# Kernel optimization log

Hardware: AMD Instinct MI355X
Metric: run time of the kernel (lower is better)

Reference implementation:

```python
import jax, jax.numpy as jnp
import numpy as np

BN_EPS = 1e-5
NORM_EPS = 1e-12  # torch F.normalize eps


def setup_inputs() -> dict:
    key = jax.random.key(0)
    ks = jax.random.split(key, 7)
    B, N, D, K = 32, 4096, 512, 64
    init_sc = 1.0 / np.sqrt(D)
    x = jax.random.normal(ks[0], (B, N, D), dtype=jnp.float32)
    clusters = init_sc * jax.random.normal(ks[1], (D, K), dtype=jnp.float32)
    clusters2 = init_sc * jax.random.normal(ks[2], (1, D, K), dtype=jnp.float32)
    bn_weight = jax.random.uniform(ks[3], (K,), dtype=jnp.float32, minval=0.5, maxval=1.5)
    bn_bias = 0.1 * jax.random.normal(ks[4], (K,), dtype=jnp.float32)
    running_mean = 0.1 * jax.random.normal(ks[5], (K,), dtype=jnp.float32)
    running_var = jax.random.uniform(ks[6], (K,), dtype=jnp.float32, minval=0.5, maxval=1.5)
    return {"x": x, "clusters": clusters, "clusters2": clusters2,
            "bn_weight": bn_weight, "bn_bias": bn_bias,
            "running_mean": running_mean, "running_var": running_var}


def reference(x, clusters, clusters2, bn_weight, bn_bias, running_mean, running_var):
    B, N, D = x.shape
    K = clusters2.shape[2]
    x_flat = x.reshape(-1, D)                              # (B*N) x D
    logits = x_flat @ clusters                             # (B*N) x (K+G)
    # BatchNorm1d in eval mode: use running stats
    inv_std = jax.lax.rsqrt(running_var + BN_EPS)
    logits = (logits - running_mean) * inv_std * bn_weight + bn_bias
    assignment = jax.nn.softmax(logits, axis=1)[:, :K]     # drop ghost clusters
    assignment = assignment.reshape(B, N, K)
    a_sum = assignment.sum(axis=1, keepdims=True)
    a = a_sum * clusters2                                  # B x D x K
    vlad = jnp.einsum('bnk,bnd->bdk', assignment, x) - a   # B x D x K
    # intra-normalization over D (torch F.normalize dim=1)
    vlad = vlad / jnp.maximum(jnp.linalg.norm(vlad, axis=1, keepdims=True), NORM_EPS)
    vlad = vlad.reshape(B, D * K)
    vlad = vlad / jnp.maximum(jnp.linalg.norm(vlad, axis=1, keepdims=True), NORM_EPS)
    return vlad
```

## Files before the change

### kernel.cpp

```cpp
#include <hip/hip_runtime.h>

#define B_ 32
#define N_ 4096
#define D_ 512
#define K_ 64

__global__ __launch_bounds__(256) void k_assign(
    const float* __restrict__ x, const float* __restrict__ clusters,
    const float* __restrict__ bnw, const float* __restrict__ bnb,
    const float* __restrict__ rm, const float* __restrict__ rv,
    float* __restrict__ asg, float* __restrict__ a_sum)
{
    const int tid = threadIdx.x;
    const int tx = tid & 15, ty = tid >> 4;
    const int r0 = blockIdx.x * 64;
    const int b  = r0 >> 12;

    __shared__ __align__(16) float xs[32][68];
    __shared__ __align__(16) float cs[32][68];
    __shared__ float red[16][64];

    float acc[4][4] = {};

    for (int k0 = 0; k0 < D_; k0 += 32) {
        #pragma unroll
        for (int l = 0; l < 2; ++l) {
            int idx = tid + (l << 8);
            int row = idx >> 3;
            int kk4 = (idx & 7) << 2;
            const float4 v = *(const float4*)&x[(size_t)(r0 + row) * D_ + k0 + kk4];
            xs[kk4 + 0][row] = v.x;
            xs[kk4 + 1][row] = v.y;
            xs[kk4 + 2][row] = v.z;
            xs[kk4 + 3][row] = v.w;
        }
        #pragma unroll
        for (int l = 0; l < 2; ++l) {
            int idx = tid + (l << 8);
            int kk  = idx >> 4;
            int c4  = (idx & 15) << 2;
            *(float4*)&cs[kk][c4] = *(const float4*)&clusters[(size_t)(k0 + kk) * K_ + c4];
        }
        __syncthreads();
        #pragma unroll
        for (int kk = 0; kk < 32; ++kk) {
            const float4 xv = *(const float4*)&xs[kk][ty << 2];
            const float4 cv = *(const float4*)&cs[kk][tx << 2];
            const float xa[4] = {xv.x, xv.y, xv.z, xv.w};
            const float ca[4] = {cv.x, cv.y, cv.z, cv.w};
            #pragma unroll
            for (int i = 0; i < 4; ++i)
                #pragma unroll
                for (int j = 0; j < 4; ++j)
                    acc[i][j] = fmaf(xa[i], ca[j], acc[i][j]);
        }
        __syncthreads();
    }

    const float4 w4 = *(const float4*)&bnw[tx << 2];
    const float4 b4 = *(const float4*)&bnb[tx << 2];
    const float4 m4 = *(const float4*)&rm[tx << 2];
    const float4 v4 = *(const float4*)&rv[tx << 2];
    const float wa[4] = {w4.x, w4.y, w4.z, w4.w};
    const float ba[4] = {b4.x, b4.y, b4.z, b4.w};
    const float ma[4] = {m4.x, m4.y, m4.z, m4.w};
    const float va[4] = {v4.x, v4.y, v4.z, v4.w};
    float alpha[4], beta[4];
    #pragma unroll
    for (int j = 0; j < 4; ++j) {
        alpha[j] = wa[j] * rsqrtf(va[j] + 1e-5f);
        beta[j]  = ba[j] - ma[j] * alpha[j];
    }

    float rs[4] = {0.f, 0.f, 0.f, 0.f};
    #pragma unroll
    for (int i = 0; i < 4; ++i) {
        float lg[4];
        #pragma unroll
        for (int j = 0; j < 4; ++j) lg[j] = fmaf(acc[i][j], alpha[j], beta[j]);
        float mx = fmaxf(fmaxf(lg[0], lg[1]), fmaxf(lg[2], lg[3]));
        #pragma unroll
        for (int msk = 1; msk <= 8; msk <<= 1) mx = fmaxf(mx, __shfl_xor(mx, msk));
        float e[4];
        float s = 0.f;
        #pragma unroll
        for (int j = 0; j < 4; ++j) { e[j] = __expf(lg[j] - mx); s += e[j]; }
        #pragma unroll
        for (int msk = 1; msk <= 8; msk <<= 1) s += __shfl_xor(s, msk);
        const float invs = 1.0f / s;
        float4 o;
        o.x = e[0] * invs; o.y = e[1] * invs; o.z = e[2] * invs; o.w = e[3] * invs;
        const int row = (ty << 2) + i;
        *(float4*)&asg[(size_t)(r0 + row) * K_ + (tx << 2)] = o;
        rs[0] += o.x; rs[1] += o.y; rs[2] += o.z; rs[3] += o.w;
    }

    *(float4*)&red[ty][tx << 2] = make_float4(rs[0], rs[1], rs[2], rs[3]);
    __syncthreads();
    if (tid < 64) {
        float s = 0.f;
        #pragma unroll
        for (int t2 = 0; t2 < 16; ++t2) s += red[t2][tid];
        atomicAdd(&a_sum[(b << 6) + tid], s);
    }
}

__global__ __launch_bounds__(256) void k_vlad(
    const float* __restrict__ x, const float* __restrict__ asg,
    float* __restrict__ part)
{
    const int tid = threadIdx.x;
    const int tx = tid & 15, ty = tid >> 4;
    const int s  = blockIdx.x;
    const int dt = blockIdx.y;
    const int b  = blockIdx.z;
    const int d0 = dt << 6;
    const int n0 = s << 10;

    __shared__ __align__(16) float xt[32][68];
    __shared__ __align__(16) float at[32][68];

    float acc[4][4] = {};

    for (int nc = 0; nc < 32; ++nc) {
        const int nb = n0 + (nc << 5);
        #pragma unroll
        for (int l = 0; l < 2; ++l) {
            int idx = tid + (l << 8);
            int nn  = idx >> 4;
            int d4  = (idx & 15) << 2;
            *(float4*)&xt[nn][d4] =
                *(const float4*)&x[(size_t)(b * N_ + nb + nn) * D_ + d0 + d4];
        }
        #pragma unroll
        for (int l = 0; l < 2; ++l) {
            int idx = tid + (l << 8);
            int nn  = idx >> 4;
            int k4  = (idx & 15) << 2;
            *(float4*)&at[nn][k4] =
                *(const float4*)&asg[(size_t)(b * N_ + nb + nn) * K_ + k4];
        }
        __syncthreads();
        #pragma unroll
        for (int nn = 0; nn < 32; ++nn) {
            const float4 xv = *(const float4*)&xt[nn][ty << 2];
            const float4 av = *(const float4*)&at[nn][tx << 2];
            const float xa[4] = {xv.x, xv.y, xv.z, xv.w};
            const float aa[4] = {av.x, av.y, av.z, av.w};
            #pragma unroll
            for (int i = 0; i < 4; ++i)
                #pragma unroll
                for (int j = 0; j < 4; ++j)
                    acc[i][j] = fmaf(xa[i], aa[j], acc[i][j]);
        }
        __syncthreads();
    }

    #pragma unroll
    for (int i = 0; i < 4; ++i) {
        const size_t off =
            ((size_t)(s * B_ + b) * D_ + d0 + (ty << 2) + i) * K_ + (tx << 2);
        *(float4*)&part[off] = make_float4(acc[i][0], acc[i][1], acc[i][2], acc[i][3]);
    }
}

__global__ __launch_bounds__(256) void k_final1(
    const float* __restrict__ part, const float* __restrict__ a_sum,
    const float* __restrict__ c2, float* __restrict__ out,
    float* __restrict__ ssqk)
{
    const int b  = blockIdx.x;
    const int dc = blockIdx.y;
    const int t  = threadIdx.x;
    const int k  = t & 63, g = t >> 6;
    __shared__ float sp[4][64];

    const float  ak = a_sum[(b << 6) + k];
    const size_t bo = (size_t)b * D_ * K_;
    const size_t PS = (size_t)B_ * D_ * K_;
    float ssq = 0.f;
    const int dlo = (dc << 7) + (g << 5);
    for (int d = dlo; d < dlo + 32; ++d) {
        const size_t off = ((size_t)d << 6) + k;
        float v = part[bo + off] + part[PS + bo + off]
                + part[2 * PS + bo + off] + part[3 * PS + bo + off];
        v = fmaf(-ak, c2[off], v);
        out[((size_t)b << 15) + off] = v;
        ssq = fmaf(v, v, ssq);
    }
    sp[g][k] = ssq;
    __syncthreads();
    if (t < 64)
        atomicAdd(&ssqk[(b << 6) + t], sp[0][t] + sp[1][t] + sp[2][t] + sp[3][t]);
}

__global__ __launch_bounds__(256) void k_final2(
    const float* __restrict__ ssqk, float* __restrict__ out)
{
    const int b  = blockIdx.x;
    const int dc = blockIdx.y;
    const int t  = threadIdx.x;
    const int k  = t & 63, g = t >> 6;
    __shared__ float invk_s[64];
    __shared__ float invg_s;

    if (t < 64) {
        const float s   = ssqk[(b << 6) + t];
        const float inv = 1.0f / fmaxf(sqrtf(s), 1e-12f);
        invk_s[t] = inv;
        float gp = s * inv * inv;
        #pragma unroll
        for (int m = 1; m < 64; m <<= 1) gp += __shfl_xor(gp, m);
        if (t == 0) invg_s = 1.0f / fmaxf(sqrtf(gp), 1e-12f);
    }
    __syncthreads();
    const float scale = invk_s[k] * invg_s;
    const int dlo = (dc << 7) + (g << 5);
    for (int d = dlo; d < dlo + 32; ++d) {
        const size_t off = ((size_t)b << 15) + ((size_t)d << 6) + k;
        out[off] *= scale;
    }
}

extern "C" void kernel_launch(void* const* d_in, const int* in_sizes, int n_in,
                              void* d_out, int out_size, void* d_ws, size_t ws_size,
                              hipStream_t stream)
{
    const float* x    = (const float*)d_in[0];
    const float* clus = (const float*)d_in[1];
    const float* c2   = (const float*)d_in[2];
    const float* bnw  = (const float*)d_in[3];
    const float* bnb  = (const float*)d_in[4];
    const float* rm   = (const float*)d_in[5];
    const float* rv   = (const float*)d_in[6];
    float* out = (float*)d_out;

    float* asg   = (float*)d_ws;
    float* a_sum = asg + (size_t)B_ * N_ * K_;
    float* ssqk  = a_sum + B_ * K_;
    float* part  = ssqk + B_ * K_;

    hipMemsetAsync(a_sum, 0, 2 * B_ * K_ * sizeof(float), stream);

    k_assign<<<dim3(B_ * N_ / 64), 256, 0, stream>>>(x, clus, bnw, bnb, rm, rv, asg, a_sum);
    k_vlad<<<dim3(4, 8, B_), 256, 0, stream>>>(x, asg, part);
    k_final1<<<dim3(B_, 4), 256, 0, stream>>>(part, a_sum, c2, out, ssqk);
    k_final2<<<dim3(B_, 4), 256, 0, stream>>>(ssqk, out);
}
```

Baseline: 543.3 us.

## Use split-bf16 MFMA for both GEMMs with transposed packed assignment buffer

```diff
diff --git a/kernel.cpp b/kernel.cpp
--- a/kernel.cpp
+++ b/kernel.cpp
@@ -1,224 +1,319 @@
 #include <hip/hip_runtime.h>
+#include <stdint.h>
 
 #define B_ 32
 #define N_ 4096
 #define D_ 512
 #define K_ 64
+#define M_ (B_ * N_)
+#define NSPLIT 8
+
+typedef float f32x4 __attribute__((ext_vector_type(4)));
+typedef short bf16x8 __attribute__((ext_vector_type(8)));
+typedef uint32_t u32;
+
+union U8 { u32 u[4]; bf16x8 v; uint4 q4; };
+
+__device__ __forceinline__ u32 pack_hi2(float a, float b) {
+    return __builtin_amdgcn_perm(__float_as_uint(b), __float_as_uint(a), 0x07060302u);
+}
+__device__ __forceinline__ u32 lo16s(u32 p0, u32 p1) {
+    return __builtin_amdgcn_perm(p1, p0, 0x05040100u);
+}
+__device__ __forceinline__ u32 hi16s(u32 p0, u32 p1) {
+    return __builtin_amdgcn_perm(p1, p0, 0x07060302u);
+}
+__device__ __forceinline__ float trunc_hi(float f) {
+    return __uint_as_float(__float_as_uint(f) & 0xffff0000u);
+}
+
+__global__ void k_prep(const float* __restrict__ clusters,
+                       bf16x8* __restrict__ cfh, bf16x8* __restrict__ cfl)
+{
+    const int t = blockIdx.x;
+    const int c = blockIdx.y;
+    const int lane = threadIdx.x;
+    const int q = lane >> 4, li = lane & 15;
+    U8 h, l;
+    #pragma unroll
+    for (int j2 = 0; j2 < 4; ++j2) {
+        float v0 = clusters[(t*32 + q*8 + 2*j2 + 0) * K_ + c*16 + li];
+        float v1 = clusters[(t*32 + q*8 + 2*j2 + 1) * K_ + c*16 + li];
+        float l0 = v0 - trunc_hi(v0), l1 = v1 - trunc_hi(v1);
+        h.u[j2] = pack_hi2(v0, v1);
+        l.u[j2] = pack_hi2(l0, l1);
+    }
+    cfh[(t*4 + c)*64 + lane] = h.v;
+    cfl[(t*4 + c)*64 + lane] = l.v;
+}
 
 __global__ __launch_bounds__(256) void k_assign(
-    const float* __restrict__ x, const float* __restrict__ clusters,
+    const float* __restrict__ x,
+    const bf16x8* __restrict__ cfh, const bf16x8* __restrict__ cfl,
     const float* __restrict__ bnw, const float* __restrict__ bnb,
     const float* __restrict__ rm, const float* __restrict__ rv,
-    float* __restrict__ asg, float* __restrict__ a_sum)
+    u32* __restrict__ asgT, float* __restrict__ a_sum)
 {
     const int tid = threadIdx.x;
-    const int tx = tid & 15, ty = tid >> 4;
-    const int r0 = blockIdx.x * 64;
-    const int b  = r0 >> 12;
-
-    __shared__ __align__(16) float xs[32][68];
-    __shared__ __align__(16) float cs[32][68];
-    __shared__ float red[16][64];
-
-    float acc[4][4] = {};
-
-    for (int k0 = 0; k0 < D_; k0 += 32) {
-        #pragma unroll
-        for (int l = 0; l < 2; ++l) {
-            int idx = tid + (l << 8);
-            int row = idx >> 3;
-            int kk4 = (idx & 7) << 2;
-            const float4 v = *(const float4*)&x[(size_t)(r0 + row) * D_ + k0 + kk4];
-            xs[kk4 + 0][row] = v.x;
-            xs[kk4 + 1][row] = v.y;
-            xs[kk4 + 2][row] = v.z;
-            xs[kk4 + 3][row] = v.w;
-        }
-        #pragma unroll
-        for (int l = 0; l < 2; ++l) {
-            int idx = tid + (l << 8);
-            int kk  = idx >> 4;
-            int c4  = (idx & 15) << 2;
-            *(float4*)&cs[kk][c4] = *(const float4*)&clusters[(size_t)(k0 + kk) * K_ + c4];
-        }
-        __syncthreads();
-        #pragma unroll
-        for (int kk = 0; kk < 32; ++kk) {
-            const float4 xv = *(const float4*)&xs[kk][ty << 2];
-            const float4 cv = *(const float4*)&cs[kk][tx << 2];
-            const float xa[4] = {xv.x, xv.y, xv.z, xv.w};
-            const float ca[4] = {cv.x, cv.y, cv.z, cv.w};
-            #pragma unroll
-            for (int i = 0; i < 4; ++i)
-                #pragma unroll
-                for (int j = 0; j < 4; ++j)
-                    acc[i][j] = fmaf(xa[i], ca[j], acc[i][j]);
-        }
-        __syncthreads();
-    }
-
-    const float4 w4 = *(const float4*)&bnw[tx << 2];
-    const float4 b4 = *(const float4*)&bnb[tx << 2];
-    const float4 m4 = *(const float4*)&rm[tx << 2];
-    const float4 v4 = *(const float4*)&rv[tx << 2];
-    const float wa[4] = {w4.x, w4.y, w4.z, w4.w};
-    const float ba[4] = {b4.x, b4.y, b4.z, b4.w};
-    const float ma[4] = {m4.x, m4.y, m4.z, m4.w};
-    const float va[4] = {v4.x, v4.y, v4.z, v4.w};
+    const int w = tid >> 6, lane = tid & 63;
+    const int q = lane >> 4, li = lane & 15;
+    const int rbase = blockIdx.x * 128 + w * 32;
+
+    __shared__ __align__(16) u32 asgT_lds[64][132];
+    __shared__ float red[4][64];
+
+    f32x4 acc[2][4];
+    #pragma unroll
+    for (int i = 0; i < 2; ++i)
+        #pragma unroll
+        for (int j = 0; j < 4; ++j) acc[i][j] = (f32x4){0.f, 0.f, 0.f, 0.f};
+
+    for (int t = 0; t < 16; ++t) {
+        bf16x8 bh[4], bl[4];
+        #pragma unroll
+        for (int c = 0; c < 4; ++c) {
+            bh[c] = cfh[(t*4 + c)*64 + lane];
+            bl[c] = cfl[(t*4 + c)*64 + lane];
+        }
+        #pragma unroll
+        for (int mt = 0; mt < 2; ++mt) {
+            const float* xp = x + (size_t)(rbase + mt*16 + li) * D_ + t*32 + q*8;
+            float v[8];
+            *(float4*)&v[0] = *(const float4*)xp;
+            *(float4*)&v[4] = *(const float4*)(xp + 4);
+            float lo[8];
+            #pragma unroll
+            for (int j = 0; j < 8; ++j) lo[j] = v[j] - trunc_hi(v[j]);
+            U8 ah, al;
+            #pragma unroll
+            for (int j2 = 0; j2 < 4; ++j2) {
+                ah.u[j2] = pack_hi2(v[2*j2], v[2*j2+1]);
+                al.u[j2] = pack_hi2(lo[2*j2], lo[2*j2+1]);
+            }
+            #pragma unroll
+            for (int c = 0; c < 4; ++c) {
+                acc[mt][c] = __builtin_amdgcn_mfma_f32_16x16x32_bf16(ah.v, bh[c], acc[mt][c], 0, 0, 0);
+                acc[mt][c] = __builtin_amdgcn_mfma_f32_16x16x32_bf16(ah.v, bl[c], acc[mt][c], 0, 0, 0);
+                acc[mt][c] = __builtin_amdgcn_mfma_f32_16x16x32_bf16(al.v, bh[c], acc[mt][c], 0, 0, 0);
+            }
+        }
+    }
+
     float alpha[4], beta[4];
     #pragma unroll
-    for (int j = 0; j < 4; ++j) {
-        alpha[j] = wa[j] * rsqrtf(va[j] + 1e-5f);
-        beta[j]  = ba[j] - ma[j] * alpha[j];
+    for (int c = 0; c < 4; ++c) {
+        const int col = c*16 + li;
+        const float a = bnw[col] * rsqrtf(rv[col] + 1e-5f);
+        alpha[c] = a;
+        beta[c]  = bnb[col] - rm[col] * a;
     }
 
     float rs[4] = {0.f, 0.f, 0.f, 0.f};
     #pragma unroll
-    for (int i = 0; i < 4; ++i) {
-        float lg[4];
-        #pragma unroll
-        for (int j = 0; j < 4; ++j) lg[j] = fmaf(acc[i][j], alpha[j], beta[j]);
-        float mx = fmaxf(fmaxf(lg[0], lg[1]), fmaxf(lg[2], lg[3]));
-        #pragma unroll
-        for (int msk = 1; msk <= 8; msk <<= 1) mx = fmaxf(mx, __shfl_xor(mx, msk));
-        float e[4];
-        float s = 0.f;
-        #pragma unroll
-        for (int j = 0; j < 4; ++j) { e[j] = __expf(lg[j] - mx); s += e[j]; }
-        #pragma unroll
-        for (int msk = 1; msk <= 8; msk <<= 1) s += __shfl_xor(s, msk);
-        const float invs = 1.0f / s;
-        float4 o;
-        o.x = e[0] * invs; o.y = e[1] * invs; o.z = e[2] * invs; o.w = e[3] * invs;
-        const int row = (ty << 2) + i;
-        *(float4*)&asg[(size_t)(r0 + row) * K_ + (tx << 2)] = o;
-        rs[0] += o.x; rs[1] += o.y; rs[2] += o.z; rs[3] += o.w;
-    }
-
-    *(float4*)&red[ty][tx << 2] = make_float4(rs[0], rs[1], rs[2], rs[3]);
+    for (int mt = 0; mt < 2; ++mt) {
+        u32 pr[4][4];
+        #pragma unroll
+        for (int reg = 0; reg < 4; ++reg) {
+            float lg[4];
+            #pragma unroll
+            for (int c = 0; c < 4; ++c) lg[c] = fmaf(acc[mt][c][reg], alpha[c], beta[c]);
+            float mx = fmaxf(fmaxf(lg[0], lg[1]), fmaxf(lg[2], lg[3]));
+            #pragma unroll
+            for (int m = 1; m <= 8; m <<= 1) mx = fmaxf(mx, __shfl_xor(mx, m));
+            float e[4], s = 0.f;
+            #pragma unroll
+            for (int c = 0; c < 4; ++c) { e[c] = __expf(lg[c] - mx); s += e[c]; }
+            #pragma unroll
+            for (int m = 1; m <= 8; m <<= 1) s += __shfl_xor(s, m);
+            const float inv = 1.0f / s;
+            #pragma unroll
+            for (int c = 0; c < 4; ++c) {
+                const float a = e[c] * inv;
+                rs[c] += a;
+                const float alo = a - trunc_hi(a);
+                pr[reg][c] = pack_hi2(a, alo);
+            }
+        }
+        #pragma unroll
+        for (int c = 0; c < 4; ++c) {
+            *(uint4*)&asgT_lds[c*16 + li][w*32 + mt*16 + q*4] =
+                make_uint4(pr[0][c], pr[1][c], pr[2][c], pr[3][c]);
+        }
+    }
+
+    #pragma unroll
+    for (int c = 0; c < 4; ++c) {
+        rs[c] += __shfl_xor(rs[c], 16);
+        rs[c] += __shfl_xor(rs[c], 32);
+    }
+    if (q == 0) {
+        #pragma unroll
+        for (int c = 0; c < 4; ++c) red[w][c*16 + li] = rs[c];
+    }
     __syncthreads();
     if (tid < 64) {
-        float s = 0.f;
-        #pragma unroll
-        for (int t2 = 0; t2 < 16; ++t2) s += red[t2][tid];
-        atomicAdd(&a_sum[(b << 6) + tid], s);
+        const float s = red[0][tid] + red[1][tid] + red[2][tid] + red[3][tid];
+        atomicAdd(&a_sum[(blockIdx.x >> 5) * K_ + tid], s);
+    }
+
+    const size_t ncol0 = (size_t)blockIdx.x * 128;
+    #pragma unroll
+    for (int l = 0; l < 8; ++l) {
+        const int ii = tid + 256*l;
+        const int k = ii >> 5, seg = ii & 31;
+        const uint4 vv = *(const uint4*)&asgT_lds[k][seg*4];
+        *(uint4*)&asgT[(size_t)k * M_ + ncol0 + seg*4] = vv;
     }
 }
 
 __global__ __launch_bounds__(256) void k_vlad(
-    const float* __restrict__ x, const float* __restrict__ asg,
+    const float* __restrict__ x, const u32* __restrict__ asgT,
     float* __restrict__ part)
 {
     const int tid = threadIdx.x;
-    const int tx = tid & 15, ty = tid >> 4;
+    const int w = tid >> 6, lane = tid & 63;
+    const int q = lane >> 4, li = lane & 15;
     const int s  = blockIdx.x;
-    const int dt = blockIdx.y;
+    const int db = blockIdx.y;
     const int b  = blockIdx.z;
-    const int d0 = dt << 6;
-    const int n0 = s << 10;
-
-    __shared__ __align__(16) float xt[32][68];
-    __shared__ __align__(16) float at[32][68];
-
-    float acc[4][4] = {};
-
-    for (int nc = 0; nc < 32; ++nc) {
-        const int nb = n0 + (nc << 5);
-        #pragma unroll
-        for (int l = 0; l < 2; ++l) {
-            int idx = tid + (l << 8);
-            int nn  = idx >> 4;
-            int d4  = (idx & 15) << 2;
-            *(float4*)&xt[nn][d4] =
-                *(const float4*)&x[(size_t)(b * N_ + nb + nn) * D_ + d0 + d4];
-        }
-        #pragma unroll
-        for (int l = 0; l < 2; ++l) {
-            int idx = tid + (l << 8);
-            int nn  = idx >> 4;
-            int k4  = (idx & 15) << 2;
-            *(float4*)&at[nn][k4] =
-                *(const float4*)&asg[(size_t)(b * N_ + nb + nn) * K_ + k4];
-        }
-        __syncthreads();
-        #pragma unroll
-        for (int nn = 0; nn < 32; ++nn) {
-            const float4 xv = *(const float4*)&xt[nn][ty << 2];
-            const float4 av = *(const float4*)&at[nn][tx << 2];
-            const float xa[4] = {xv.x, xv.y, xv.z, xv.w};
-            const float aa[4] = {av.x, av.y, av.z, av.w};
-            #pragma unroll
-            for (int i = 0; i < 4; ++i)
-                #pragma unroll
-                for (int j = 0; j < 4; ++j)
-                    acc[i][j] = fmaf(xa[i], aa[j], acc[i][j]);
-        }
-        __syncthreads();
-    }
-
+    const int d0 = db*256 + w*64;
+    const int nbb = b * N_ + s * (N_ / NSPLIT);
+
+    f32x4 acc[4][4];
+    #pragma unroll
+    for (int i = 0; i < 4; ++i)
+        #pragma unroll
+        for (int j = 0; j < 4; ++j) acc[i][j] = (f32x4){0.f, 0.f, 0.f, 0.f};
+
+    for (int ch = 0; ch < (N_ / NSPLIT) / 32; ++ch) {
+        const int nb = ch*32 + q*8;
+        bf16x8 ah[4], al[4];
+        #pragma unroll
+        for (int mt = 0; mt < 4; ++mt) {
+            const u32* ap = asgT + (size_t)(mt*16 + li) * M_ + nbb + nb;
+            u32 p[8];
+            *(uint4*)&p[0] = *(const uint4*)ap;
+            *(uint4*)&p[4] = *(const uint4*)(ap + 4);
+            U8 uh, ul;
+            #pragma unroll
+            for (int j2 = 0; j2 < 4; ++j2) {
+                uh.u[j2] = lo16s(p[2*j2], p[2*j2+1]);
+                ul.u[j2] = hi16s(p[2*j2], p[2*j2+1]);
+            }
+            ah[mt] = uh.v; al[mt] = ul.v;
+        }
+        #pragma unroll
+        for (int nt = 0; nt < 4; ++nt) {
+            const float* xp = x + (size_t)(nbb + nb) * D_ + d0 + nt*16 + li;
+            float v[8];
+            #pragma unroll
+            for (int j = 0; j < 8; ++j) v[j] = xp[(size_t)j * D_];
+            float lo[8];
+            #pragma unroll
+            for (int j = 0; j < 8; ++j) lo[j] = v[j] - trunc_hi(v[j]);
+            U8 bh, bl;
+            #pragma unroll
+            for (int j2 = 0; j2 < 4; ++j2) {
+                bh.u[j2] = pack_hi2(v[2*j2], v[2*j2+1]);
+                bl.u[j2] = pack_hi2(lo[2*j2], lo[2*j2+1]);
+            }
+            #pragma unroll
+            for (int mt = 0; mt < 4; ++mt) {
+                acc[mt][nt] = __builtin_amdgcn_mfma_f32_16x16x32_bf16(ah[mt], bh.v, acc[mt][nt], 0, 0, 0);
+                acc[mt][nt] = __builtin_amdgcn_mfma_f32_16x16x32_bf16(ah[mt], bl.v, acc[mt][nt], 0, 0, 0);
+                acc[mt][nt] = __builtin_amdgcn_mfma_f32_16x16x32_bf16(al[mt], bh.v, acc[mt][nt], 0, 0, 0);
+            }
+        }
+    }
+
+    float* pp = part + ((size_t)s * B_ + b) * ((size_t)K_ * D_);
+    #pragma unroll
+    for (int mt = 0; mt < 4; ++mt)
+        #pragma unroll
+        for (int nt = 0; nt < 4; ++nt) {
+            const int d = d0 + nt*16 + li;
+            #pragma unroll
+            for (int reg = 0; reg < 4; ++reg) {
+                const int k = mt*16 + q*4 + reg;
+                pp[(size_t)k * D_ + d] = acc[mt][nt][reg];
+            }
+        }
+}
+
+__global__ __launch_bounds__(256) void k_final1(
+    const float* __restrict__ part_ro, const float* __restrict__ a_sum,
+    const float* __restrict__ c2, float* __restrict__ part0,
+    float* __restrict__ ssqk)
+{
+    const int b = blockIdx.x, dc = blockIdx.y;
+    const int tid = threadIdx.x;
+    const int k = tid >> 2, ds = tid & 3;
+    const int d0 = dc*64 + ds*16;
+    const float ak = a_sum[b*K_ + k];
+    const size_t PS = (size_t)B_ * K_ * D_;
+    const size_t base = ((size_t)b * K_ + k) * D_ + d0;
+    float ssq = 0.f;
     #pragma unroll
     for (int i = 0; i < 4; ++i) {
-        const size_t off =
-            ((size_t)(s * B_ + b) * D_ + d0 + (ty << 2) + i) * K_ + (tx << 2);
-        *(float4*)&part[off] = make_float4(acc[i][0], acc[i][1], acc[i][2], acc[i][3]);
-    }
-}
-
-__global__ __launch_bounds__(256) void k_final1(
-    const float* __restrict__ part, const float* __restrict__ a_sum,
-    const float* __restrict__ c2, float* __restrict__ out,
-    float* __restrict__ ssqk)
-{
-    const int b  = blockIdx.x;
-    const int dc = blockIdx.y;
-    const int t  = threadIdx.x;
-    const int k  = t & 63, g = t >> 6;
-    __shared__ float sp[4][64];
-
-    const float  ak = a_sum[(b << 6) + k];
-    const size_t bo = (size_t)b * D_ * K_;
-    const size_t PS = (size_t)B_ * D_ * K_;
-    float ssq = 0.f;
-    const int dlo = (dc << 7) + (g << 5);
-    for (int d = dlo; d < dlo + 32; ++d) {
-        const size_t off = ((size_t)d << 6) + k;
-        float v = part[bo + off] + part[PS + bo + off]
-                + part[2 * PS + bo + off] + part[3 * PS + bo + off];
-        v = fmaf(-ak, c2[off], v);
-        out[((size_t)b << 15) + off] = v;
-        ssq = fmaf(v, v, ssq);
-    }
-    sp[g][k] = ssq;
+        float4 v = *(const float4*)(part_ro + base + i*4);
+        #pragma unroll
+        for (int s = 1; s < NSPLIT; ++s) {
+            const float4 p = *(const float4*)(part_ro + s*PS + base + i*4);
+            v.x += p.x; v.y += p.y; v.z += p.z; v.w += p.w;
+        }
+        const int d = d0 + i*4;
+        v.x = fmaf(-ak, c2[(d+0)*K_ + k], v.x);
+        v.y = fmaf(-ak, c2[(d+1)*K_ + k], v.y);
+        v.z = fmaf(-ak, c2[(d+2)*K_ + k], v.z);
+        v.w = fmaf(-ak, c2[(d+3)*K_ + k], v.w);
+        ssq = fmaf(v.x, v.x, fmaf(v.y, v.y, fmaf(v.z, v.z, fmaf(v.w, v.w, ssq))));
+        *(float4*)(part0 + base + i*4) = v;
+    }
+    ssq += __shfl_xor(ssq, 1);
+    ssq += __shfl_xor(ssq, 2);
+    if (ds == 0) atomicAdd(&ssqk[b*K_ + k], ssq);
+}
+
+__global__ __launch_bounds__(256) void k_final2(
+    const float* __restrict__ v0, const float* __restrict__ ssqk,
+    float* __restrict__ out)
+{
+    const int b = blockIdx.x, dc = blockIdx.y;
+    const int tid = threadIdx.x;
+    __shared__ float T[64][65];
+    __shared__ float invk[64];
+    __shared__ float invg_s;
+
+    if (tid < 64) {
+        const float ss = ssqk[b*K_ + tid];
+        const float inv = 1.0f / fmaxf(sqrtf(ss), 1e-12f);
+        invk[tid] = inv;
+        float gp = ss * inv * inv;
+        #pragma unroll
+        for (int m = 1; m < 64; m <<= 1) gp += __shfl_xor(gp, m);
+        if (tid == 0) invg_s = 1.0f / fmaxf(sqrtf(gp), 1e-12f);
+    }
     __syncthreads();
-    if (t < 64)
-        atomicAdd(&ssqk[(b << 6) + t], sp[0][t] + sp[1][t] + sp[2][t] + sp[3][t]);
-}
-
-__global__ __launch_bounds__(256) void k_final2(
-    const float* __restrict__ ssqk, float* __restrict__ out)
-{
-    const int b  = blockIdx.x;
-    const int dc = blockIdx.y;
-    const int t  = threadIdx.x;
-    const int k  = t & 63, g = t >> 6;
-    __shared__ float invk_s[64];
-    __shared__ float invg_s;
-
-    if (t < 64) {
-        const float s   = ssqk[(b << 6) + t];
-        const float inv = 1.0f / fmaxf(sqrtf(s), 1e-12f);
-        invk_s[t] = inv;
-        float gp = s * inv * inv;
-        #pragma unroll
-        for (int m = 1; m < 64; m <<= 1) gp += __shfl_xor(gp, m);
-        if (t == 0) invg_s = 1.0f / fmaxf(sqrtf(gp), 1e-12f);
+
+    const int k = tid >> 2, ds = tid & 3;
+    const float sc = invk[k] * invg_s;
+    const size_t base = ((size_t)b * K_ + k) * D_ + dc*64 + ds*16;
+    #pragma unroll
+    for (int i = 0; i < 4; ++i) {
+        float4 v = *(const float4*)(v0 + base + i*4);
+        const int dd = ds*16 + i*4;
+        T[k][dd+0] = v.x * sc;
+        T[k][dd+1] = v.y * sc;
+        T[k][dd+2] = v.z * sc;
+        T[k][dd+3] = v.w * sc;
     }
     __syncthreads();
-    const float scale = invk_s[k] * invg_s;
-    const int dlo = (dc << 7) + (g << 5);
-    for (int d = dlo; d < dlo + 32; ++d) {
-        const size_t off = ((size_t)b << 15) + ((size_t)d << 6) + k;
-        out[off] *= scale;
+
+    const int k2 = tid & 63, dl = tid >> 6;
+    #pragma unroll
+    for (int i = 0; i < 16; ++i) {
+        const int dd = dl*16 + i;
+        out[((size_t)b * D_ + dc*64 + dd) * K_ + k2] = T[k2][dd];
     }
 }
 
@@ -235,15 +330,18 @@
     const float* rv   = (const float*)d_in[6];
     float* out = (float*)d_out;
 
-    float* asg   = (float*)d_ws;
-    float* a_sum = asg + (size_t)B_ * N_ * K_;
+    u32*   asgT  = (u32*)d_ws;
+    float* part  = (float*)(asgT + (size_t)K_ * M_);
+    float* a_sum = part + (size_t)NSPLIT * B_ * K_ * D_;
     float* ssqk  = a_sum + B_ * K_;
-    float* part  = ssqk + B_ * K_;
+    bf16x8* cfh  = (bf16x8*)(ssqk + B_ * K_);
+    bf16x8* cfl  = cfh + 16*4*64;
 
     hipMemsetAsync(a_sum, 0, 2 * B_ * K_ * sizeof(float), stream);
 
-    k_assign<<<dim3(B_ * N_ / 64), 256, 0, stream>>>(x, clus, bnw, bnb, rm, rv, asg, a_sum);
-    k_vlad<<<dim3(4, 8, B_), 256, 0, stream>>>(x, asg, part);
-    k_final1<<<dim3(B_, 4), 256, 0, stream>>>(part, a_sum, c2, out, ssqk);
-    k_final2<<<dim3(B_, 4), 256, 0, stream>>>(ssqk, out);
-}
+    k_prep<<<dim3(16, 4), 64, 0, stream>>>(clus, cfh, cfl);
+    k_assign<<<dim3(M_ / 128), 256, 0, stream>>>(x, cfh, cfl, bnw, bnb, rm, rv, asgT, a_sum);
+    k_vlad<<<dim3(NSPLIT, 2, B_), 256, 0, stream>>>(x, asgT, part);
+    k_final1<<<dim3(B_, 8), 256, 0, stream>>>(part, a_sum, c2, part, ssqk);
+    k_final2<<<dim3(B_, 8), 256, 0, stream>>>(part, ssqk, out);
+}
```

New measurement: 464.7 us (median of 2 runs). -14.5%, faster.
